# Performance work log

Hardware: AMD Instinct MI355X
Metric: run time of the kernel (lower is better)

## Reference

```python
import jax, jax.numpy as jnp
import numpy as np

B, T, D, N, L = 8, 2048, 256, 64, 4
LN_EPS = 1e-5


def setup_inputs() -> dict:
    key = jax.random.key(0)
    ks = jax.random.split(key, 8)
    def rn(k, shape, scale=1.0):
        return jax.random.normal(k, shape, dtype=jnp.float32) * scale
    A_init = jnp.log(0.5 + jnp.arange(N, dtype=jnp.float32))  # (N,)
    inp = {
        "sequences": rn(ks[0], (B, T, D)),
        # per-layer stacked params (leading dim L)
        "Wi": rn(ks[1], (L, D, D), 1.0 / np.sqrt(D)),
        "bi": jnp.zeros((L, D), jnp.float32),
        "A_log": jnp.broadcast_to(A_init, (L, D, N)) + 0.0,
        "Cm": rn(ks[2], (L, D, N), 1.0 / np.sqrt(N)),
        "Dp": jnp.ones((L, D), jnp.float32),
        "log_dt": jax.random.uniform(ks[3], (L, D), jnp.float32) * (np.log(0.1) - np.log(0.001)) + np.log(0.001),
        "Wo": rn(ks[4], (L, D, D), 1.0 / np.sqrt(D)),
        "bo": jnp.zeros((L, D), jnp.float32),
        "ln1_g": jnp.ones((L, D), jnp.float32),
        "ln1_b": jnp.zeros((L, D), jnp.float32),
        "ln2_g": jnp.ones((L, D), jnp.float32),
        "ln2_b": jnp.zeros((L, D), jnp.float32),
        "W1": rn(ks[5], (L, D, 4 * D), 1.0 / np.sqrt(D)),
        "b1": jnp.zeros((L, 4 * D), jnp.float32),
        "W2": rn(ks[6], (L, 4 * D, D), 1.0 / np.sqrt(4 * D)),
        "b2": jnp.zeros((L, D), jnp.float32),
        "lnf_g": jnp.ones((D,), jnp.float32),
        "lnf_b": jnp.zeros((D,), jnp.float32),
    }
    return inp


def _ln(x, g, b):
    m = x.mean(-1, keepdims=True)
    v = x.var(-1, keepdims=True)
    return (x - m) / jnp.sqrt(v + LN_EPS) * g + b


def _s4_kernel(A_log_l, Cm_l, log_dt_l, Tlen):
    dt = jnp.exp(log_dt_l)                       # (D,)
    A = -jnp.exp(A_log_l)                        # (D,N)
    A_bar = jnp.exp(A * dt[:, None])             # (D,N)
    B_bar = (A_bar - 1.0) / (A * np.sqrt(N))     # (D,N)
    CB = Cm_l * B_bar                            # (D,N)
    logAb = jnp.log(jnp.clip(A_bar, 1e-10))
    powers = jnp.arange(Tlen, dtype=jnp.float32)
    # (D,N,T) power tensor contracted over N -> (D,T)
    return jnp.einsum('dn,dnt->dt', CB, jnp.exp(logAb[:, :, None] * powers))


def reference(sequences, Wi, bi, A_log, Cm, Dp, log_dt, Wo, bo,
              ln1_g, ln1_b, ln2_g, ln2_b, W1, b1, W2, b2, lnf_g, lnf_b):
    x = sequences  # dropout is identity in eval mode
    Tlen = x.shape[1]
    nfft = 2 * Tlen
    for l in range(L):
        # --- S4D sub-block (pre-norm) ---
        h = _ln(x, ln1_g[l], ln1_b[l])
        u = (h @ Wi[l] + bi[l]).transpose(0, 2, 1)   # (B,D,T)
        K = _s4_kernel(A_log[l], Cm[l], log_dt[l], Tlen)  # (D,T)
        u_f = jnp.fft.rfft(u, n=nfft, axis=-1)
        K_f = jnp.fft.rfft(K, n=nfft, axis=-1)
        y = jnp.fft.irfft(u_f * K_f[None], n=nfft, axis=-1)[..., :Tlen]
        y = y + Dp[l][None, :, None] * u
        y = y.transpose(0, 2, 1) @ Wo[l] + bo[l]
        x = x + y
        # --- MLP sub-block (pre-norm) ---
        h2 = _ln(x, ln2_g[l], ln2_b[l])
        x = x + (jax.nn.gelu(h2 @ W1[l] + b1[l], approximate=False) @ W2[l] + b2[l])
    return _ln(x, lnf_g, lnf_b)
```

## Files before the change

kernel.cpp:

```cpp
#include <hip/hip_runtime.h>
#include <hip/hip_bf16.h>

#define NB 8
#define TT 2048
#define DD 256
#define NN 64
#define LL 4
#define CC 32
#define GG 64
#define BT (NB*TT)

typedef __attribute__((ext_vector_type(8))) short short8;
typedef __attribute__((ext_vector_type(4))) short short4v;
typedef __attribute__((ext_vector_type(4))) float f32x4;

__device__ __forceinline__ float bf2f(__hip_bfloat16 v){ return __bfloat162float(v); }
__device__ __forceinline__ __hip_bfloat16 f2bf(float v){ return __float2bfloat16(v); }
__device__ __forceinline__ short f2bfbits(float v){
  __hip_bfloat16 h = __float2bfloat16(v);
  return __builtin_bit_cast(short, h);
}
__device__ __forceinline__ float bfbits2f(short s){
  __hip_bfloat16 h = __builtin_bit_cast(__hip_bfloat16, s);
  return __bfloat162float(h);
}

__device__ __forceinline__ int get_bf(const void* dtp){
  unsigned u = *(const unsigned*)dtp;
  return ((u >> 16) == (u & 0xFFFFu)) ? 1 : 0;
}

__device__ __forceinline__ float ldin(const void* p, size_t i, int bf){
  return bf ? __bfloat162float(((const __hip_bfloat16*)p)[i]) : ((const float*)p)[i];
}

__device__ __forceinline__ float gelu_f(float x){
  float y = 0.79788456f * fmaf(0.044715f, x*x*x, x);
  float e = __expf(-2.0f * fabsf(y));
  float t = (1.0f - e) / (1.0f + e);
  t = (y >= 0.0f) ? t : -t;
  return 0.5f * x * (1.0f + t);
}

__device__ __forceinline__ void async16(const void* g, void* l){
  __builtin_amdgcn_global_load_lds(
      (const __attribute__((address_space(1))) void*)(unsigned long long)g,
      (__attribute__((address_space(3))) void*)(unsigned long long)l,
      16, 0, 0);
}

__global__ __launch_bounds__(256) void cast_ln_kernel(const void* __restrict__ seq,
    __hip_bfloat16* __restrict__ x, __hip_bfloat16* __restrict__ hN,
    const void* __restrict__ g, const void* __restrict__ b,
    const void* __restrict__ dtp)
{
  int bf = get_bf(dtp);
  int lane = threadIdx.x & 63, w = threadIdx.x >> 6;
  int row = blockIdx.x * 4 + w;
  int c = lane * 4;
  size_t base = (size_t)row*DD + c;
  float v0 = ldin(seq, base+0, bf), v1 = ldin(seq, base+1, bf);
  float v2 = ldin(seq, base+2, bf), v3 = ldin(seq, base+3, bf);
  short4v xk; xk.x=f2bfbits(v0); xk.y=f2bfbits(v1); xk.z=f2bfbits(v2); xk.w=f2bfbits(v3);
  *(short4v*)(x + base) = xk;
  float s = v0+v1+v2+v3;
  #pragma unroll
  for (int o = 1; o < 64; o <<= 1) s += __shfl_xor(s, o);
  float mean = s * (1.0f/DD);
  float d0=v0-mean, d1=v1-mean, d2=v2-mean, d3=v3-mean;
  float sq = d0*d0+d1*d1+d2*d2+d3*d3;
  #pragma unroll
  for (int o = 1; o < 64; o <<= 1) sq += __shfl_xor(sq, o);
  float r = rsqrtf(sq * (1.0f/DD) + 1e-5f);
  short4v hk;
  hk.x = f2bfbits(d0*r*ldin(g,c+0,bf) + ldin(b,c+0,bf));
  hk.y = f2bfbits(d1*r*ldin(g,c+1,bf) + ldin(b,c+1,bf));
  hk.z = f2bfbits(d2*r*ldin(g,c+2,bf) + ldin(b,c+2,bf));
  hk.w = f2bfbits(d3*r*ldin(g,c+3,bf) + ldin(b,c+3,bf));
  *(short4v*)(hN + base) = hk;
}

__global__ __launch_bounds__(256) void transpose_all_kernel(
    const void* __restrict__ Wi, const void* __restrict__ Wo,
    const void* __restrict__ W1, const void* __restrict__ W2,
    __hip_bfloat16* __restrict__ WiT, __hip_bfloat16* __restrict__ WoT,
    __hip_bfloat16* __restrict__ W1T, __hip_bfloat16* __restrict__ W2T,
    const void* __restrict__ dtp)
{
  int bf = get_bf(dtp);
  __shared__ float tile[32][33];
  int id = blockIdx.x;
  const void* W; __hip_bfloat16* Wt; int K, N, l, n0, k0;
  if (id < 256){
    W=Wi; Wt=WiT; K=DD; N=DD;
    int t=id;       l=t>>6; int r=t&63;  n0=(r&7)*32;  k0=(r>>3)*32;
  } else if (id < 512){
    W=Wo; Wt=WoT; K=DD; N=DD;
    int t=id-256;   l=t>>6; int r=t&63;  n0=(r&7)*32;  k0=(r>>3)*32;
  } else if (id < 1536){
    W=W1; Wt=W1T; K=DD; N=4*DD;
    int t=id-512;   l=t>>8; int r=t&255; n0=(r&31)*32; k0=(r>>5)*32;
  } else {
    W=W2; Wt=W2T; K=4*DD; N=DD;
    int t=id-1536;  l=t>>8; int r=t&255; n0=(r&7)*32;  k0=(r>>3)*32;
  }
  size_t zoff = (size_t)l * K * N;
  int tx = threadIdx.x, ty = threadIdx.y;
  #pragma unroll
  for (int i = 0; i < 4; i++)
    tile[ty + i*8][tx] = ldin(W, zoff + (size_t)(k0 + ty + i*8)*N + n0 + tx, bf);
  __syncthreads();
  #pragma unroll
  for (int i = 0; i < 4; i++)
    Wt[zoff + (size_t)(n0 + ty + i*8)*K + k0 + tx] = f2bf(tile[tx][ty + i*8]);
}

__global__ __launch_bounds__(256) void gemm_w1_kernel(
    const __hip_bfloat16* __restrict__ A, const __hip_bfloat16* __restrict__ Wt,
    const void* __restrict__ bias, size_t boff,
    __hip_bfloat16* __restrict__ C, int N, int K, const void* __restrict__ dtp)
{
  int bf = get_bf(dtp);
  __shared__ __align__(16) char smem[24576];
  short (*Als)[128][32] = (short(*)[128][32])smem;
  short (*Bls)[64][32]  = (short(*)[64][32])(smem + 16384);
  short* Cls = (short*)smem;
  int tid = threadIdx.x;
  int lane = tid & 63, w = tid >> 6;
  int quad = lane >> 4, row16 = lane & 15;
  int wm = (w >> 1) * 64, wn = (w & 1) * 32;
  int bm = blockIdx.x * 128, bn = blockIdx.y * 64;
  const short* Ag = (const short*)A + (size_t)bm * K;
  const short* Bg = (const short*)Wt + (size_t)bn * K;
  int r0 = tid >> 2, c8 = (tid & 3) * 8;
  f32x4 acc[4][2] = {};
  for (int k0 = 0; k0 < K; k0 += 64){
    #pragma unroll
    for (int kc = 0; kc < 2; kc++){
      async16(Ag + (size_t)r0*K      + k0 + kc*32 + c8, &Als[kc][r0][c8]);
      async16(Ag + (size_t)(64+r0)*K + k0 + kc*32 + c8, &Als[kc][64+r0][c8]);
      async16(Bg + (size_t)r0*K      + k0 + kc*32 + c8, &Bls[kc][r0][c8]);
    }
    __syncthreads();
    #pragma unroll
    for (int kc = 0; kc < 2; kc++){
      short8 af[4], bfr[2];
      #pragma unroll
      for (int i = 0; i < 4; i++)
        af[i] = *(const short8*)&Als[kc][wm + i*16 + row16][quad*8];
      #pragma unroll
      for (int j = 0; j < 2; j++)
        bfr[j] = *(const short8*)&Bls[kc][wn + j*16 + row16][quad*8];
      #pragma unroll
      for (int i = 0; i < 4; i++)
        #pragma unroll
        for (int j = 0; j < 2; j++)
          acc[i][j] = __builtin_amdgcn_mfma_f32_16x16x32_bf16(af[i], bfr[j], acc[i][j], 0, 0, 0);
    }
    __syncthreads();
  }
  #pragma unroll
  for (int i = 0; i < 4; i++){
    #pragma unroll
    for (int j = 0; j < 2; j++){
      int col = wn + j*16 + row16;
      float bv = ldin(bias, boff + bn + col, bf);
      #pragma unroll
      for (int r = 0; r < 4; r++){
        int row = wm + i*16 + quad*4 + r;
        Cls[row*72 + col] = f2bfbits(gelu_f(acc[i][j][r] + bv));
      }
    }
  }
  __syncthreads();
  #pragma unroll
  for (int p = 0; p < 4; p++){
    int ch = p*256 + tid;
    int row = ch >> 3, c0 = (ch & 7) * 8;
    short8 v = *(const short8*)&Cls[row*72 + c0];
    *(short8*)&C[(size_t)(bm + row)*N + bn + c0] = v;
  }
}

__global__ __launch_bounds__(256) void gemm_wi_lf_kernel(
    const __hip_bfloat16* __restrict__ A, const __hip_bfloat16* __restrict__ Wt,
    const void* __restrict__ bias, size_t boff,
    __hip_bfloat16* __restrict__ uout, __hip_bfloat16* __restrict__ LFS,
    const float* __restrict__ abT, int K, const void* __restrict__ dtp)
{
  int bf = get_bf(dtp);
  __shared__ __align__(16) char smem[73728];
  short (*Als)[32][32]  = (short(*)[32][32])smem;
  short (*Bls)[256][32] = (short(*)[256][32])(smem + 8192);
  float* Cls = (float*)smem;
  int tid = threadIdx.x, lane = tid & 63, w = tid >> 6;
  int quad = lane >> 4, row16 = lane & 15;
  int wn = w * 64;
  int bm = blockIdx.x * 32;
  const short* Ag = (const short*)A + (size_t)bm * K;
  const short* Bg = (const short*)Wt;
  f32x4 acc[2][4] = {};
  for (int k0 = 0; k0 < K; k0 += 128){
    #pragma unroll
    for (int p = 0; p < 2; p++){
      int ch = p*256 + tid;
      int kc = ch >> 7, r = (ch >> 2) & 31, c = (ch & 3) * 8;
      async16(Ag + (size_t)r*K + k0 + kc*32 + c, &Als[kc][r][c]);
    }
    #pragma unroll
    for (int p = 0; p < 16; p++){
      int ch = p*256 + tid;
      int kc = ch >> 10, r = (ch >> 2) & 255, c = (ch & 3) * 8;
      async16(Bg + (size_t)r*K + k0 + kc*32 + c, &Bls[kc][r][c]);
    }
    __syncthreads();
    #pragma unroll
    for (int kc = 0; kc < 4; kc++){
      short8 af[2], bfr[4];
      #pragma unroll
      for (int i = 0; i < 2; i++)
        af[i] = *(const short8*)&Als[kc][i*16 + row16][quad*8];
      #pragma unroll
      for (int j = 0; j < 4; j++)
        bfr[j] = *(const short8*)&Bls[kc][wn + j*16 + row16][quad*8];
      #pragma unroll
      for (int i = 0; i < 2; i++)
        #pragma unroll
        for (int j = 0; j < 4; j++)
          acc[i][j] = __builtin_amdgcn_mfma_f32_16x16x32_bf16(af[i], bfr[j], acc[i][j], 0, 0, 0);
    }
    __syncthreads();
  }
  #pragma unroll
  for (int i = 0; i < 2; i++)
    #pragma unroll
    for (int j = 0; j < 4; j++){
      int col = wn + j*16 + row16;
      #pragma unroll
      for (int r = 0; r < 4; r++){
        int row = i*16 + quad*4 + r;
        Cls[row*260 + col] = acc[i][j][r];
      }
    }
  __syncthreads();
  {
    int row = tid >> 3, l7 = tid & 7;
    size_t rbase = (size_t)(bm + row)*DD;
    #pragma unroll
    for (int q = 0; q < 8; q++){
      int c0 = l7*4 + q*32;
      float4 t = *(const float4*)&Cls[row*260 + c0];
      float v0 = t.x + ldin(bias, boff+c0+0, bf);
      float v1 = t.y + ldin(bias, boff+c0+1, bf);
      float v2 = t.z + ldin(bias, boff+c0+2, bf);
      float v3 = t.w + ldin(bias, boff+c0+3, bf);
      float4 wbk; wbk.x=v0; wbk.y=v1; wbk.z=v2; wbk.w=v3;
      *(float4*)&Cls[row*260 + c0] = wbk;
      short4v pk; pk.x=f2bfbits(v0); pk.y=f2bfbits(v1); pk.z=f2bfbits(v2); pk.w=f2bfbits(v3);
      *(short4v*)&uout[rbase + c0] = pk;
    }
  }
  __syncthreads();
  {
    int d = tid;
    int cix = bm >> 5;
    float ab[NN], accn[NN];
    #pragma unroll
    for (int n = 0; n < NN; n++){ ab[n] = abT[n*DD + d]; accn[n] = 0.0f; }
    #pragma unroll 1
    for (int s = 0; s < CC; s++){
      float uv = Cls[s*260 + d];
      #pragma unroll
      for (int n = 0; n < NN; n++) accn[n] = fmaf(ab[n], accn[n], uv);
    }
    #pragma unroll
    for (int n = 0; n < NN; n++)
      LFS[((size_t)cix*NN + n)*DD + d] = f2bf(accn[n]);
  }
}

__global__ __launch_bounds__(256) void s4_scan_kernel(__hip_bfloat16* __restrict__ LFS,
    const float* __restrict__ AbarCT)
{
  int d = threadIdx.x;
  int n = blockIdx.x & (NN-1), b = blockIdx.x >> 6;
  float a = AbarCT[n*DD + d];
  size_t base = ((size_t)(b*GG)*NN + n)*DD + d;
  const size_t gs = (size_t)NN*DD;
  float s = 0.0f;
  #pragma unroll 1
  for (int g = 0; g < GG; g += 4){
    size_t i0 = base + (size_t)(g+0)*gs;
    size_t i1 = base + (size_t)(g+1)*gs;
    size_t i2 = base + (size_t)(g+2)*gs;
    size_t i3 = base + (size_t)(g+3)*gs;
    float lf0 = bf2f(LFS[i0]);
    float lf1 = bf2f(LFS[i1]);
    float lf2 = bf2f(LFS[i2]);
    float lf3 = bf2f(LFS[i3]);
    LFS[i0] = f2bf(s); s = fmaf(a, s, lf0);
    LFS[i1] = f2bf(s); s = fmaf(a, s, lf1);
    LFS[i2] = f2bf(s); s = fmaf(a, s, lf2);
    LFS[i3] = f2bf(s); s = fmaf(a, s, lf3);
  }
}

__global__ __launch_bounds__(512, 4) void gemm_wo_recur_kernel(
    const __hip_bfloat16* __restrict__ uB, const __hip_bfloat16* __restrict__ Sin,
    const float* __restrict__ abT, const float* __restrict__ cbT,
    const void* __restrict__ Dp, size_t dpoff,
    const __hip_bfloat16* __restrict__ Wt, const void* __restrict__ bias, size_t boff,
    const __hip_bfloat16* __restrict__ resx, __hip_bfloat16* __restrict__ xout,
    const void* __restrict__ g, size_t goff, const void* __restrict__ bb, size_t bboff,
    __hip_bfloat16* __restrict__ hout, int K)
{
  int bf = get_bf(Dp);
  __shared__ __align__(16) char smem[65536];
  short* Uls   = (short*)smem;
  short* Afull = (short*)(smem + 16384);
  short (*Bls)[256][32] = (short(*)[256][32])(smem + 32768);
  float* Cls = (float*)smem;
  int tid = threadIdx.x, lane = tid & 63, w = tid >> 6;
  int quad = lane >> 4, row16 = lane & 15;
  int bm = blockIdx.x * 32;
  {
    const short* ug = (const short*)uB + (size_t)bm * DD;
    async16(ug + tid*8,        Uls + tid*8);
    async16(ug + 4096 + tid*8, Uls + 4096 + tid*8);
  }
  int d = tid >> 1, ng = tid & 1, nb = ng * 32;
  float st[32], ab[32], cb[32];
  {
    const __hip_bfloat16* sbase = Sin + ((size_t)(bm >> 5) * NN + nb)*DD + d;
    const float* abase = abT + (size_t)nb*DD + d;
    const float* cbase = cbT + (size_t)nb*DD + d;
    #pragma unroll
    for (int i = 0; i < 32; i++){
      st[i] = bf2f(sbase[(size_t)i*DD]);
      ab[i] = abase[(size_t)i*DD];
      cb[i] = cbase[(size_t)i*DD];
    }
  }
  float dp = ldin(Dp, dpoff + d, bf);
  __syncthreads();
  {
    short* ya = Afull + (d >> 5)*1024 + (d & 31);
    #pragma unroll 1
    for (int tau = 0; tau < CC; tau++){
      float uv = bfbits2f(Uls[tau*DD + d]);
      float a0 = 0.0f, a1 = 0.0f, a2 = 0.0f, a3 = 0.0f;
      #pragma unroll
      for (int i = 0; i < 32; i += 4){
        st[i+0] = fmaf(ab[i+0], st[i+0], uv); a0 = fmaf(cb[i+0], st[i+0], a0);
        st[i+1] = fmaf(ab[i+1], st[i+1], uv); a1 = fmaf(cb[i+1], st[i+1], a1);
        st[i+2] = fmaf(ab[i+2], st[i+2], uv); a2 = fmaf(cb[i+2], st[i+2], a2);
        st[i+3] = fmaf(ab[i+3], st[i+3], uv); a3 = fmaf(cb[i+3], st[i+3], a3);
      }
      float tot = (a0 + a1) + (a2 + a3);
      tot += __shfl_xor(tot, 1);
      if (ng == 0) ya[tau*32] = f2bfbits(fmaf(dp, uv, tot));
    }
  }
  __syncthreads();
  const short* Bg = (const short*)Wt;
  int wn = w * 32;
  f32x4 acc[2][2] = {};
  for (int k0 = 0; k0 < K; k0 += 64){
    #pragma unroll
    for (int p = 0; p < 4; p++){
      int ch = p*512 + tid;
      int kc = ch >> 10, rem = ch & 1023, r = rem >> 2, c = (rem & 3) * 8;
      async16(Bg + (size_t)r*K + k0 + kc*32 + c, &Bls[kc][r][c]);
    }
    __syncthreads();
    #pragma unroll
    for (int kc = 0; kc < 2; kc++){
      short8 af[2], bfr[2];
      #pragma unroll
      for (int i = 0; i < 2; i++)
        af[i] = *(const short8*)&Afull[((k0 >> 5) + kc)*1024 + (i*16 + row16)*32 + quad*8];
      #pragma unroll
      for (int j = 0; j < 2; j++)
        bfr[j] = *(const short8*)&Bls[kc][wn + j*16 + row16][quad*8];
      #pragma unroll
      for (int i = 0; i < 2; i++)
        #pragma unroll
        for (int j = 0; j < 2; j++)
          acc[i][j] = __builtin_amdgcn_mfma_f32_16x16x32_bf16(af[i], bfr[j], acc[i][j], 0, 0, 0);
    }
    __syncthreads();
  }
  #pragma unroll
  for (int i = 0; i < 2; i++)
    #pragma unroll
    for (int j = 0; j < 2; j++){
      int col = wn + j*16 + row16;
      #pragma unroll
      for (int r = 0; r < 4; r++){
        int row = i*16 + quad*4 + r;
        Cls[row*260 + col] = acc[i][j][r];
      }
    }
  __syncthreads();
  int row = tid >> 4, l4 = tid & 15;
  size_t rbase = (size_t)(bm + row)*DD;
  float v[4][4];
  #pragma unroll
  for (int q = 0; q < 4; q++){
    int c0 = l4*4 + q*64;
    float4 t = *(const float4*)&Cls[row*260 + c0];
    short4v rx = *(const short4v*)&resx[rbase + c0];
    v[q][0] = t.x + ldin(bias, boff+c0+0, bf) + bfbits2f(rx.x);
    v[q][1] = t.y + ldin(bias, boff+c0+1, bf) + bfbits2f(rx.y);
    v[q][2] = t.z + ldin(bias, boff+c0+2, bf) + bfbits2f(rx.z);
    v[q][3] = t.w + ldin(bias, boff+c0+3, bf) + bfbits2f(rx.w);
    short4v pk; pk.x=f2bfbits(v[q][0]); pk.y=f2bfbits(v[q][1]);
    pk.z=f2bfbits(v[q][2]); pk.w=f2bfbits(v[q][3]);
    *(short4v*)&xout[rbase + c0] = pk;
  }
  float s = 0.0f, sq = 0.0f;
  #pragma unroll
  for (int q = 0; q < 4; q++)
    #pragma unroll
    for (int e = 0; e < 4; e++){ s += v[q][e]; sq += v[q][e]*v[q][e]; }
  #pragma unroll
  for (int o = 1; o < 16; o <<= 1){ s += __shfl_xor(s, o); sq += __shfl_xor(sq, o); }
  float mean = s * (1.0f/DD);
  float rstd = rsqrtf(sq * (1.0f/DD) - mean*mean + 1e-5f);
  #pragma unroll
  for (int q = 0; q < 4; q++){
    int c0 = l4*4 + q*64;
    short4v pk;
    pk.x = f2bfbits((v[q][0]-mean)*rstd*ldin(g,goff+c0+0,bf) + ldin(bb,bboff+c0+0,bf));
    pk.y = f2bfbits((v[q][1]-mean)*rstd*ldin(g,goff+c0+1,bf) + ldin(bb,bboff+c0+1,bf));
    pk.z = f2bfbits((v[q][2]-mean)*rstd*ldin(g,goff+c0+2,bf) + ldin(bb,bboff+c0+2,bf));
    pk.w = f2bfbits((v[q][3]-mean)*rstd*ldin(g,goff+c0+3,bf) + ldin(bb,bboff+c0+3,bf));
    *(short4v*)&hout[rbase + c0] = pk;
  }
}

template <int MODE>
__global__ __launch_bounds__(256) void gemm_row_kernel(
    const __hip_bfloat16* __restrict__ A, const __hip_bfloat16* __restrict__ Wt,
    const void* __restrict__ bias, size_t boff,
    const __hip_bfloat16* __restrict__ resx, __hip_bfloat16* __restrict__ xout,
    const void* __restrict__ g, size_t goff,
    const void* __restrict__ bb, size_t bboff,
    __hip_bfloat16* __restrict__ hout, void* __restrict__ vout,
    int K, const void* __restrict__ dtp)
{
  int bf = get_bf(dtp);
  __shared__ __align__(16) char smem[73728];
  short (*Als)[32][32]  = (short(*)[32][32])smem;
  short (*Bls)[256][32] = (short(*)[256][32])(smem + 8192);
  float* Cls = (float*)smem;
  int tid = threadIdx.x, lane = tid & 63, w = tid >> 6;
  int quad = lane >> 4, row16 = lane & 15;
  int wn = w * 64;
  int bm = blockIdx.x * 32;
  const short* Ag = (const short*)A + (size_t)bm * K;
  const short* Bg = (const short*)Wt;
  f32x4 acc[2][4] = {};
  for (int k0 = 0; k0 < K; k0 += 128){
    #pragma unroll
    for (int p = 0; p < 2; p++){
      int ch = p*256 + tid;
      int kc = ch >> 7, r = (ch >> 2) & 31, c = (ch & 3) * 8;
      async16(Ag + (size_t)r*K + k0 + kc*32 + c, &Als[kc][r][c]);
    }
    #pragma unroll
    for (int p = 0; p < 16; p++){
      int ch = p*256 + tid;
      int kc = ch >> 10, r = (ch >> 2) & 255, c = (ch & 3) * 8;
      async16(Bg + (size_t)r*K + k0 + kc*32 + c, &Bls[kc][r][c]);
    }
    __syncthreads();
    #pragma unroll
    for (int kc = 0; kc < 4; kc++){
      short8 af[2], bfr[4];
      #pragma unroll
      for (int i = 0; i < 2; i++)
        af[i] = *(const short8*)&Als[kc][i*16 + row16][quad*8];
      #pragma unroll
      for (int j = 0; j < 4; j++)
        bfr[j] = *(const short8*)&Bls[kc][wn + j*16 + row16][quad*8];
      #pragma unroll
      for (int i = 0; i < 2; i++)
        #pragma unroll
        for (int j = 0; j < 4; j++)
          acc[i][j] = __builtin_amdgcn_mfma_f32_16x16x32_bf16(af[i], bfr[j], acc[i][j], 0, 0, 0);
    }
    __syncthreads();
  }
  #pragma unroll
  for (int i = 0; i < 2; i++)
    #pragma unroll
    for (int j = 0; j < 4; j++){
      int col = wn + j*16 + row16;
      #pragma unroll
      for (int r = 0; r < 4; r++){
        int row = i*16 + quad*4 + r;
        Cls[row*260 + col] = acc[i][j][r];
      }
    }
  __syncthreads();
  int row = tid >> 3, l7 = tid & 7;
  size_t rbase = (size_t)(bm + row)*DD;
  float v[8][4];
  #pragma unroll
  for (int q = 0; q < 8; q++){
    int c0 = l7*4 + q*32;
    float4 t = *(const float4*)&Cls[row*260 + c0];
    short4v rx = *(const short4v*)&resx[rbase + c0];
    v[q][0] = t.x + ldin(bias, boff+c0+0, bf) + bfbits2f(rx.x);
    v[q][1] = t.y + ldin(bias, boff+c0+1, bf) + bfbits2f(rx.y);
    v[q][2] = t.z + ldin(bias, boff+c0+2, bf) + bfbits2f(rx.z);
    v[q][3] = t.w + ldin(bias, boff+c0+3, bf) + bfbits2f(rx.w);
    if (MODE == 1){
      short4v pk; pk.x=f2bfbits(v[q][0]); pk.y=f2bfbits(v[q][1]);
      pk.z=f2bfbits(v[q][2]); pk.w=f2bfbits(v[q][3]);
      *(short4v*)&xout[rbase + c0] = pk;
    }
  }
  float s = 0.0f, sq = 0.0f;
  #pragma unroll
  for (int q = 0; q < 8; q++)
    #pragma unroll
    for (int e = 0; e < 4; e++){ s += v[q][e]; sq += v[q][e]*v[q][e]; }
  #pragma unroll
  for (int o = 1; o < 8; o <<= 1){ s += __shfl_xor(s, o); sq += __shfl_xor(sq, o); }
  float mean = s * (1.0f/DD);
  float rstd = rsqrtf(sq * (1.0f/DD) - mean*mean + 1e-5f);
  #pragma unroll
  for (int q = 0; q < 8; q++){
    int c0 = l7*4 + q*32;
    float o0 = (v[q][0]-mean)*rstd*ldin(g,goff+c0+0,bf) + ldin(bb,bboff+c0+0,bf);
    float o1 = (v[q][1]-mean)*rstd*ldin(g,goff+c0+1,bf) + ldin(bb,bboff+c0+1,bf);
    float o2 = (v[q][2]-mean)*rstd*ldin(g,goff+c0+2,bf) + ldin(bb,bboff+c0+2,bf);
    float o3 = (v[q][3]-mean)*rstd*ldin(g,goff+c0+3,bf) + ldin(bb,bboff+c0+3,bf);
    if (MODE == 1){
      short4v pk; pk.x=f2bfbits(o0); pk.y=f2bfbits(o1); pk.z=f2bfbits(o2); pk.w=f2bfbits(o3);
      *(short4v*)&hout[rbase + c0] = pk;
    } else {
      if (bf){
        short4v pk; pk.x=f2bfbits(o0); pk.y=f2bfbits(o1); pk.z=f2bfbits(o2); pk.w=f2bfbits(o3);
        *(short4v*)&((__hip_bfloat16*)vout)[rbase + c0] = pk;
      } else {
        float4 pk; pk.x=o0; pk.y=o1; pk.z=o2; pk.w=o3;
        *(float4*)&((float*)vout)[rbase + c0] = pk;
      }
    }
  }
}

__global__ __launch_bounds__(256) void s4_setup_kernel(const void* __restrict__ A_log,
    const void* __restrict__ Cm, const void* __restrict__ log_dt,
    float* __restrict__ AbarT, float* __restrict__ AbarCT, float* __restrict__ cbT,
    const void* __restrict__ dtp)
{
  int bf = get_bf(dtp);
  int d = threadIdx.x, n = blockIdx.x, l = blockIdx.y;
  float dtv = expf(ldin(log_dt, (size_t)l*DD + d, bf));
  float A   = -expf(ldin(A_log, ((size_t)l*DD + d)*NN + n, bf));
  float ab  = expf(A * dtv);
  float bbv = (fabsf(A) > 1e-8f) ? (ab - 1.0f) / (A * 8.0f) : dtv * 0.125f;
  float cb  = ldin(Cm, ((size_t)l*DD + d)*NN + n, bf) * bbv;
  size_t o = ((size_t)l*NN + n)*DD + d;
  AbarT[o] = ab;
  cbT[o]   = cb;
  float p = ab;
  #pragma unroll
  for (int i = 0; i < 5; i++) p *= p;
  AbarCT[o] = p;
}

extern "C" void kernel_launch(void* const* d_in, const int* in_sizes, int n_in,
                              void* d_out, int out_size, void* d_ws, size_t ws_size,
                              hipStream_t stream) {
  const void* seq   = d_in[0];
  const void* Wi    = d_in[1];
  const void* bi    = d_in[2];
  const void* A_log = d_in[3];
  const void* Cm    = d_in[4];
  const void* Dp    = d_in[5];
  const void* logdt = d_in[6];
  const void* Wo    = d_in[7];
  const void* bo    = d_in[8];
  const void* ln1g  = d_in[9];
  const void* ln1b  = d_in[10];
  const void* ln2g  = d_in[11];
  const void* ln2b  = d_in[12];
  const void* W1    = d_in[13];
  const void* b1    = d_in[14];
  const void* W2    = d_in[15];
  const void* b2    = d_in[16];
  const void* lnfg  = d_in[17];
  const void* lnfb  = d_in[18];

  char* ws = (char*)d_ws;
  size_t off = 0;
  __hip_bfloat16* x   = (__hip_bfloat16*)(ws + off); off += (size_t)BT*DD*2;
  __hip_bfloat16* uB  = (__hip_bfloat16*)(ws + off); off += (size_t)BT*DD*2;
  __hip_bfloat16* hN  = (__hip_bfloat16*)(ws + off); off += (size_t)BT*DD*2;
  __hip_bfloat16* mid = (__hip_bfloat16*)(ws + off); off += (size_t)BT*4*DD*2;
  __hip_bfloat16* LFS = (__hip_bfloat16*)(ws + off); off += (size_t)NB*GG*NN*DD*2;
  __hip_bfloat16* WiT = (__hip_bfloat16*)(ws + off); off += (size_t)LL*DD*DD*2;
  __hip_bfloat16* WoT = (__hip_bfloat16*)(ws + off); off += (size_t)LL*DD*DD*2;
  __hip_bfloat16* W1T = (__hip_bfloat16*)(ws + off); off += (size_t)LL*DD*4*DD*2;
  __hip_bfloat16* W2T = (__hip_bfloat16*)(ws + off); off += (size_t)LL*4*DD*DD*2;
  float* AbarT  = (float*)(ws + off); off += (size_t)LL*NN*DD*4;
  float* AbarCT = (float*)(ws + off); off += (size_t)LL*NN*DD*4;
  float* cbT    = (float*)(ws + off); off += (size_t)LL*NN*DD*4;

  (void)in_sizes; (void)n_in; (void)out_size; (void)ws_size;

  cast_ln_kernel<<<BT/4, 256, 0, stream>>>(seq, x, hN, ln1g, ln1b, Dp);
  transpose_all_kernel<<<2560, dim3(32,8), 0, stream>>>(
      Wi, Wo, W1, W2, WiT, WoT, W1T, W2T, Dp);
  s4_setup_kernel<<<dim3(NN, LL), DD, 0, stream>>>(A_log, Cm, logdt, AbarT, AbarCT, cbT, Dp);

  for (int l = 0; l < LL; l++){
    const size_t oD  = (size_t)l*DD;
    const size_t o4D = (size_t)l*4*DD;
    const float* abT  = AbarT  + (size_t)l*NN*DD;
    const float* abCT = AbarCT + (size_t)l*NN*DD;
    const float* cbTl = cbT    + (size_t)l*NN*DD;

    gemm_wi_lf_kernel<<<BT/32, 256, 0, stream>>>(
        hN, WiT + (size_t)l*DD*DD, bi, oD, uB, LFS, abT, DD, Dp);
    s4_scan_kernel<<<NB*NN, 256, 0, stream>>>(LFS, abCT);
    gemm_wo_recur_kernel<<<BT/32, 512, 0, stream>>>(
        uB, LFS, abT, cbTl, Dp, oD,
        WoT + (size_t)l*DD*DD, bo, oD, x, x,
        ln2g, oD, ln2b, oD, hN, DD);

    gemm_w1_kernel<<<dim3(BT/128, 4*DD/64), 256, 0, stream>>>(
        hN, W1T + (size_t)l*DD*4*DD, b1, o4D, mid, 4*DD, DD, Dp);
    if (l < LL-1){
      gemm_row_kernel<1><<<BT/32, 256, 0, stream>>>(
          mid, W2T + (size_t)l*4*DD*DD, b2, oD, x, x,
          ln1g, (size_t)(l+1)*DD, ln1b, (size_t)(l+1)*DD, hN, nullptr, 4*DD, Dp);
    } else {
      gemm_row_kernel<2><<<BT/32, 256, 0, stream>>>(
          mid, W2T + (size_t)l*4*DD*DD, b2, oD, x, nullptr,
          lnfg, 0, lnfb, 0, nullptr, d_out, 4*DD, Dp);
    }
  }
}
```

Measured before the change: 616.7 us.

## Split fused recurrence+Wo GEMM into separate recurrence and row-GEMM kernels

Unfuses the chunked S4 recurrence from the Wo projection. The recurrence kernel now writes y to a global scratch buffer (reusing the mid buffer), and the existing gemm_row_kernel<1> does Wo, bias, residual and LN2. The goal is to shrink the recurrence kernel's shared memory (only the U tile remains) so more blocks can run at once, and to reuse the tuned GEMM path. The cost is an extra kernel launch plus a global round trip of y.

```diff
diff --git a/kernel.cpp b/kernel.cpp
--- a/kernel.cpp
+++ b/kernel.cpp
@@ -305,24 +305,16 @@
   }
 }
 
-__global__ __launch_bounds__(512, 4) void gemm_wo_recur_kernel(
+__global__ __launch_bounds__(512, 4) void recur_kernel(
     const __hip_bfloat16* __restrict__ uB, const __hip_bfloat16* __restrict__ Sin,
     const float* __restrict__ abT, const float* __restrict__ cbT,
     const void* __restrict__ Dp, size_t dpoff,
-    const __hip_bfloat16* __restrict__ Wt, const void* __restrict__ bias, size_t boff,
-    const __hip_bfloat16* __restrict__ resx, __hip_bfloat16* __restrict__ xout,
-    const void* __restrict__ g, size_t goff, const void* __restrict__ bb, size_t bboff,
-    __hip_bfloat16* __restrict__ hout, int K)
+    __hip_bfloat16* __restrict__ yout)
 {
   int bf = get_bf(Dp);
-  __shared__ __align__(16) char smem[65536];
-  short* Uls   = (short*)smem;
-  short* Afull = (short*)(smem + 16384);
-  short (*Bls)[256][32] = (short(*)[256][32])(smem + 32768);
-  float* Cls = (float*)smem;
-  int tid = threadIdx.x, lane = tid & 63, w = tid >> 6;
-  int quad = lane >> 4, row16 = lane & 15;
-  int bm = blockIdx.x * 32;
+  __shared__ __align__(16) short Uls[CC*DD];
+  int tid = threadIdx.x;
+  int bm = blockIdx.x * CC;
   {
     const short* ug = (const short*)uB + (size_t)bm * DD;
     async16(ug + tid*8,        Uls + tid*8);
@@ -343,99 +335,23 @@
   }
   float dp = ldin(Dp, dpoff + d, bf);
   __syncthreads();
-  {
-    short* ya = Afull + (d >> 5)*1024 + (d & 31);
-    #pragma unroll 1
-    for (int tau = 0; tau < CC; tau++){
-      float uv = bfbits2f(Uls[tau*DD + d]);
-      float a0 = 0.0f, a1 = 0.0f, a2 = 0.0f, a3 = 0.0f;
-      #pragma unroll
-      for (int i = 0; i < 32; i += 4){
-        st[i+0] = fmaf(ab[i+0], st[i+0], uv); a0 = fmaf(cb[i+0], st[i+0], a0);
-        st[i+1] = fmaf(ab[i+1], st[i+1], uv); a1 = fmaf(cb[i+1], st[i+1], a1);
-        st[i+2] = fmaf(ab[i+2], st[i+2], uv); a2 = fmaf(cb[i+2], st[i+2], a2);
-        st[i+3] = fmaf(ab[i+3], st[i+3], uv); a3 = fmaf(cb[i+3], st[i+3], a3);
-      }
-      float tot = (a0 + a1) + (a2 + a3);
-      tot += __shfl_xor(tot, 1);
-      if (ng == 0) ya[tau*32] = f2bfbits(fmaf(dp, uv, tot));
-    }
-  }
-  __syncthreads();
-  const short* Bg = (const short*)Wt;
-  int wn = w * 32;
-  f32x4 acc[2][2] = {};
-  for (int k0 = 0; k0 < K; k0 += 64){
-    #pragma unroll
-    for (int p = 0; p < 4; p++){
-      int ch = p*512 + tid;
-      int kc = ch >> 10, rem = ch & 1023, r = rem >> 2, c = (rem & 3) * 8;
-      async16(Bg + (size_t)r*K + k0 + kc*32 + c, &Bls[kc][r][c]);
-    }
-    __syncthreads();
-    #pragma unroll
-    for (int kc = 0; kc < 2; kc++){
-      short8 af[2], bfr[2];
-      #pragma unroll
-      for (int i = 0; i < 2; i++)
-        af[i] = *(const short8*)&Afull[((k0 >> 5) + kc)*1024 + (i*16 + row16)*32 + quad*8];
-      #pragma unroll
-      for (int j = 0; j < 2; j++)
-        bfr[j] = *(const short8*)&Bls[kc][wn + j*16 + row16][quad*8];
-      #pragma unroll
-      for (int i = 0; i < 2; i++)
-        #pragma unroll
-        for (int j = 0; j < 2; j++)
-          acc[i][j] = __builtin_amdgcn_mfma_f32_16x16x32_bf16(af[i], bfr[j], acc[i][j], 0, 0, 0);
-    }
-    __syncthreads();
-  }
-  #pragma unroll
-  for (int i = 0; i < 2; i++)
-    #pragma unroll
-    for (int j = 0; j < 2; j++){
-      int col = wn + j*16 + row16;
-      #pragma unroll
-      for (int r = 0; r < 4; r++){
-        int row = i*16 + quad*4 + r;
-        Cls[row*260 + col] = acc[i][j][r];
-      }
-    }
-  __syncthreads();
-  int row = tid >> 4, l4 = tid & 15;
-  size_t rbase = (size_t)(bm + row)*DD;
-  float v[4][4];
-  #pragma unroll
-  for (int q = 0; q < 4; q++){
-    int c0 = l4*4 + q*64;
-    float4 t = *(const float4*)&Cls[row*260 + c0];
-    short4v rx = *(const short4v*)&resx[rbase + c0];
-    v[q][0] = t.x + ldin(bias, boff+c0+0, bf) + bfbits2f(rx.x);
-    v[q][1] = t.y + ldin(bias, boff+c0+1, bf) + bfbits2f(rx.y);
-    v[q][2] = t.z + ldin(bias, boff+c0+2, bf) + bfbits2f(rx.z);
-    v[q][3] = t.w + ldin(bias, boff+c0+3, bf) + bfbits2f(rx.w);
-    short4v pk; pk.x=f2bfbits(v[q][0]); pk.y=f2bfbits(v[q][1]);
-    pk.z=f2bfbits(v[q][2]); pk.w=f2bfbits(v[q][3]);
-    *(short4v*)&xout[rbase + c0] = pk;
-  }
-  float s = 0.0f, sq = 0.0f;
-  #pragma unroll
-  for (int q = 0; q < 4; q++)
-    #pragma unroll
-    for (int e = 0; e < 4; e++){ s += v[q][e]; sq += v[q][e]*v[q][e]; }
-  #pragma unroll
-  for (int o = 1; o < 16; o <<= 1){ s += __shfl_xor(s, o); sq += __shfl_xor(sq, o); }
-  float mean = s * (1.0f/DD);
-  float rstd = rsqrtf(sq * (1.0f/DD) - mean*mean + 1e-5f);
-  #pragma unroll
-  for (int q = 0; q < 4; q++){
-    int c0 = l4*4 + q*64;
-    short4v pk;
-    pk.x = f2bfbits((v[q][0]-mean)*rstd*ldin(g,goff+c0+0,bf) + ldin(bb,bboff+c0+0,bf));
-    pk.y = f2bfbits((v[q][1]-mean)*rstd*ldin(g,goff+c0+1,bf) + ldin(bb,bboff+c0+1,bf));
-    pk.z = f2bfbits((v[q][2]-mean)*rstd*ldin(g,goff+c0+2,bf) + ldin(bb,bboff+c0+2,bf));
-    pk.w = f2bfbits((v[q][3]-mean)*rstd*ldin(g,goff+c0+3,bf) + ldin(bb,bboff+c0+3,bf));
-    *(short4v*)&hout[rbase + c0] = pk;
+  __hip_bfloat16* ya = yout + (size_t)bm*DD + d;
+  float uv = bfbits2f(Uls[d]);
+  #pragma unroll 1
+  for (int tau = 0; tau < CC; tau++){
+    float uvn = (tau < CC-1) ? bfbits2f(Uls[(tau+1)*DD + d]) : 0.0f;
+    float a0 = 0.0f, a1 = 0.0f, a2 = 0.0f, a3 = 0.0f;
+    #pragma unroll
+    for (int i = 0; i < 32; i += 4){
+      st[i+0] = fmaf(ab[i+0], st[i+0], uv); a0 = fmaf(cb[i+0], st[i+0], a0);
+      st[i+1] = fmaf(ab[i+1], st[i+1], uv); a1 = fmaf(cb[i+1], st[i+1], a1);
+      st[i+2] = fmaf(ab[i+2], st[i+2], uv); a2 = fmaf(cb[i+2], st[i+2], a2);
+      st[i+3] = fmaf(ab[i+3], st[i+3], uv); a3 = fmaf(cb[i+3], st[i+3], a3);
+    }
+    float tot = (a0 + a1) + (a2 + a3);
+    tot += __shfl_xor(tot, 1);
+    if (ng == 0) ya[(size_t)tau*DD] = f2bf(fmaf(dp, uv, tot));
+    uv = uvn;
   }
 }
 
@@ -612,6 +528,8 @@
   float* AbarCT = (float*)(ws + off); off += (size_t)LL*NN*DD*4;
   float* cbT    = (float*)(ws + off); off += (size_t)LL*NN*DD*4;
 
+  __hip_bfloat16* yC = mid;
+
   (void)in_sizes; (void)n_in; (void)out_size; (void)ws_size;
 
   cast_ln_kernel<<<BT/4, 256, 0, stream>>>(seq, x, hN, ln1g, ln1b, Dp);
@@ -629,10 +547,11 @@
     gemm_wi_lf_kernel<<<BT/32, 256, 0, stream>>>(
         hN, WiT + (size_t)l*DD*DD, bi, oD, uB, LFS, abT, DD, Dp);
     s4_scan_kernel<<<NB*NN, 256, 0, stream>>>(LFS, abCT);
-    gemm_wo_recur_kernel<<<BT/32, 512, 0, stream>>>(
-        uB, LFS, abT, cbTl, Dp, oD,
-        WoT + (size_t)l*DD*DD, bo, oD, x, x,
-        ln2g, oD, ln2b, oD, hN, DD);
+    recur_kernel<<<BT/32, 512, 0, stream>>>(
+        uB, LFS, abT, cbTl, Dp, oD, yC);
+    gemm_row_kernel<1><<<BT/32, 256, 0, stream>>>(
+        yC, WoT + (size_t)l*DD*DD, bo, oD, x, x,
+        ln2g, oD, ln2b, oD, hN, nullptr, DD, Dp);
 
     gemm_w1_kernel<<<dim3(BT/128, 4*DD/64), 256, 0, stream>>>(
         hN, W1T + (size_t)l*DD*4*DD, b1, o4D, mid, 4*DD, DD, Dp);
```

Result: slower. 643.0 us (+4.3%).

## Double-buffer GEMM k-tiles and prefetch Wo tiles during the scan recurrence

Applied to the files above, without the earlier changes.

The Wi and W2 row GEMMs now use ping-pong LDS buffers with 64-wide k-tiles, so the loads for tile t+1 are issued while tile t is computed. The Wo GEMM inside the recurrence kernel loads its first weight tile during the scan and then alternates between the freed U buffer and a new buffer. Its LDS footprint shrinks, which may let more blocks fit per CU. The scan loop also prefetches the next u value one step ahead. The cost is more barrier iterations with less work between them.

```diff
diff --git a/kernel.cpp b/kernel.cpp
--- a/kernel.cpp
+++ b/kernel.cpp
@@ -190,8 +190,8 @@
 {
   int bf = get_bf(dtp);
   __shared__ __align__(16) char smem[73728];
-  short (*Als)[32][32]  = (short(*)[32][32])smem;
-  short (*Bls)[256][32] = (short(*)[256][32])(smem + 8192);
+  short (*Als)[2][32][32]  = (short(*)[2][32][32])smem;
+  short (*Bls)[2][256][32] = (short(*)[2][256][32])(smem + 8192);
   float* Cls = (float*)smem;
   int tid = threadIdx.x, lane = tid & 63, w = tid >> 6;
   int quad = lane >> 4, row16 = lane & 15;
@@ -199,30 +199,39 @@
   int bm = blockIdx.x * 32;
   const short* Ag = (const short*)A + (size_t)bm * K;
   const short* Bg = (const short*)Wt;
+  int nt = K >> 6;
+  {
+    int ch = tid; int kc = ch>>7, r=(ch>>2)&31, c=(ch&3)*8;
+    async16(Ag + (size_t)r*K + kc*32 + c, &Als[0][kc][r][c]);
+    #pragma unroll
+    for (int p = 0; p < 8; p++){
+      int c2 = p*256 + tid; int k2 = c2>>10, r2=(c2>>2)&255, cc=(c2&3)*8;
+      async16(Bg + (size_t)r2*K + k2*32 + cc, &Bls[0][k2][r2][cc]);
+    }
+  }
+  __syncthreads();
   f32x4 acc[2][4] = {};
-  for (int k0 = 0; k0 < K; k0 += 128){
-    #pragma unroll
-    for (int p = 0; p < 2; p++){
-      int ch = p*256 + tid;
-      int kc = ch >> 7, r = (ch >> 2) & 31, c = (ch & 3) * 8;
-      async16(Ag + (size_t)r*K + k0 + kc*32 + c, &Als[kc][r][c]);
-    }
-    #pragma unroll
-    for (int p = 0; p < 16; p++){
-      int ch = p*256 + tid;
-      int kc = ch >> 10, r = (ch >> 2) & 255, c = (ch & 3) * 8;
-      async16(Bg + (size_t)r*K + k0 + kc*32 + c, &Bls[kc][r][c]);
-    }
-    __syncthreads();
-    #pragma unroll
-    for (int kc = 0; kc < 4; kc++){
+  for (int t = 0; t < nt; t++){
+    int cur = t & 1;
+    if (t + 1 < nt){
+      int nb_ = cur ^ 1, k0 = (t+1) << 6;
+      int ch = tid; int kc = ch>>7, r=(ch>>2)&31, c=(ch&3)*8;
+      async16(Ag + (size_t)r*K + k0 + kc*32 + c, &Als[nb_][kc][r][c]);
+      #pragma unroll
+      for (int p = 0; p < 8; p++){
+        int c2 = p*256 + tid; int k2 = c2>>10, r2=(c2>>2)&255, cc=(c2&3)*8;
+        async16(Bg + (size_t)r2*K + k0 + k2*32 + cc, &Bls[nb_][k2][r2][cc]);
+      }
+    }
+    #pragma unroll
+    for (int kc = 0; kc < 2; kc++){
       short8 af[2], bfr[4];
       #pragma unroll
       for (int i = 0; i < 2; i++)
-        af[i] = *(const short8*)&Als[kc][i*16 + row16][quad*8];
+        af[i] = *(const short8*)&Als[cur][kc][i*16 + row16][quad*8];
       #pragma unroll
       for (int j = 0; j < 4; j++)
-        bfr[j] = *(const short8*)&Bls[kc][wn + j*16 + row16][quad*8];
+        bfr[j] = *(const short8*)&Bls[cur][kc][wn + j*16 + row16][quad*8];
       #pragma unroll
       for (int i = 0; i < 2; i++)
         #pragma unroll
@@ -312,21 +321,27 @@
     const __hip_bfloat16* __restrict__ Wt, const void* __restrict__ bias, size_t boff,
     const __hip_bfloat16* __restrict__ resx, __hip_bfloat16* __restrict__ xout,
     const void* __restrict__ g, size_t goff, const void* __restrict__ bb, size_t bboff,
-    __hip_bfloat16* __restrict__ hout, int K)
+    __hip_bfloat16* __restrict__ hout)
 {
   int bf = get_bf(Dp);
-  __shared__ __align__(16) char smem[65536];
+  __shared__ __align__(16) char smem[50176];
   short* Uls   = (short*)smem;
   short* Afull = (short*)(smem + 16384);
-  short (*Bls)[256][32] = (short(*)[256][32])(smem + 32768);
-  float* Cls = (float*)smem;
+  short* Bext  = (short*)(smem + 32768);
+  float* Cls   = (float*)(smem + 16384);
   int tid = threadIdx.x, lane = tid & 63, w = tid >> 6;
   int quad = lane >> 4, row16 = lane & 15;
-  int bm = blockIdx.x * 32;
+  int bm = blockIdx.x * CC;
+  const short* Bg = (const short*)Wt;
   {
     const short* ug = (const short*)uB + (size_t)bm * DD;
     async16(ug + tid*8,        Uls + tid*8);
     async16(ug + 4096 + tid*8, Uls + 4096 + tid*8);
+    #pragma unroll
+    for (int p = 0; p < 2; p++){
+      int ch = p*512 + tid; int r = ch >> 2, c = (ch & 3) * 8;
+      async16(Bg + (size_t)r*DD + c, Bext + ch*8);
+    }
   }
   int d = tid >> 1, ng = tid & 1, nb = ng * 32;
   float st[32], ab[32], cb[32];
@@ -345,9 +360,10 @@
   __syncthreads();
   {
     short* ya = Afull + (d >> 5)*1024 + (d & 31);
+    float uv = bfbits2f(Uls[d]);
     #pragma unroll 1
     for (int tau = 0; tau < CC; tau++){
-      float uv = bfbits2f(Uls[tau*DD + d]);
+      float uvn = (tau < CC-1) ? bfbits2f(Uls[(tau+1)*DD + d]) : 0.0f;
       float a0 = 0.0f, a1 = 0.0f, a2 = 0.0f, a3 = 0.0f;
       #pragma unroll
       for (int i = 0; i < 32; i += 4){
@@ -359,35 +375,35 @@
       float tot = (a0 + a1) + (a2 + a3);
       tot += __shfl_xor(tot, 1);
       if (ng == 0) ya[tau*32] = f2bfbits(fmaf(dp, uv, tot));
-    }
-  }
-  __syncthreads();
-  const short* Bg = (const short*)Wt;
+      uv = uvn;
+    }
+  }
+  __syncthreads();
   int wn = w * 32;
   f32x4 acc[2][2] = {};
-  for (int k0 = 0; k0 < K; k0 += 64){
-    #pragma unroll
-    for (int p = 0; p < 4; p++){
-      int ch = p*512 + tid;
-      int kc = ch >> 10, rem = ch & 1023, r = rem >> 2, c = (rem & 3) * 8;
-      async16(Bg + (size_t)r*K + k0 + kc*32 + c, &Bls[kc][r][c]);
-    }
-    __syncthreads();
-    #pragma unroll
-    for (int kc = 0; kc < 2; kc++){
-      short8 af[2], bfr[2];
-      #pragma unroll
-      for (int i = 0; i < 2; i++)
-        af[i] = *(const short8*)&Afull[((k0 >> 5) + kc)*1024 + (i*16 + row16)*32 + quad*8];
+  #pragma unroll
+  for (int t = 0; t < 8; t++){
+    if (t < 7){
+      short* nxt = ((t+1) & 1) ? Uls : Bext;
+      #pragma unroll
+      for (int p = 0; p < 2; p++){
+        int ch = p*512 + tid; int r = ch >> 2, c = (ch & 3) * 8;
+        async16(Bg + (size_t)r*DD + (t+1)*32 + c, nxt + ch*8);
+      }
+    }
+    const short* cur = (t & 1) ? Uls : Bext;
+    short8 af[2], bfr[2];
+    #pragma unroll
+    for (int i = 0; i < 2; i++)
+      af[i] = *(const short8*)&Afull[t*1024 + (i*16 + row16)*32 + quad*8];
+    #pragma unroll
+    for (int j = 0; j < 2; j++)
+      bfr[j] = *(const short8*)&cur[(wn + j*16 + row16)*32 + quad*8];
+    #pragma unroll
+    for (int i = 0; i < 2; i++)
       #pragma unroll
       for (int j = 0; j < 2; j++)
-        bfr[j] = *(const short8*)&Bls[kc][wn + j*16 + row16][quad*8];
-      #pragma unroll
-      for (int i = 0; i < 2; i++)
-        #pragma unroll
-        for (int j = 0; j < 2; j++)
-          acc[i][j] = __builtin_amdgcn_mfma_f32_16x16x32_bf16(af[i], bfr[j], acc[i][j], 0, 0, 0);
-    }
+        acc[i][j] = __builtin_amdgcn_mfma_f32_16x16x32_bf16(af[i], bfr[j], acc[i][j], 0, 0, 0);
     __syncthreads();
   }
   #pragma unroll
@@ -451,8 +467,8 @@
 {
   int bf = get_bf(dtp);
   __shared__ __align__(16) char smem[73728];
-  short (*Als)[32][32]  = (short(*)[32][32])smem;
-  short (*Bls)[256][32] = (short(*)[256][32])(smem + 8192);
+  short (*Als)[2][32][32]  = (short(*)[2][32][32])smem;
+  short (*Bls)[2][256][32] = (short(*)[2][256][32])(smem + 8192);
   float* Cls = (float*)smem;
   int tid = threadIdx.x, lane = tid & 63, w = tid >> 6;
   int quad = lane >> 4, row16 = lane & 15;
@@ -460,30 +476,39 @@
   int bm = blockIdx.x * 32;
   const short* Ag = (const short*)A + (size_t)bm * K;
   const short* Bg = (const short*)Wt;
+  int nt = K >> 6;
+  {
+    int ch = tid; int kc = ch>>7, r=(ch>>2)&31, c=(ch&3)*8;
+    async16(Ag + (size_t)r*K + kc*32 + c, &Als[0][kc][r][c]);
+    #pragma unroll
+    for (int p = 0; p < 8; p++){
+      int c2 = p*256 + tid; int k2 = c2>>10, r2=(c2>>2)&255, cc=(c2&3)*8;
+      async16(Bg + (size_t)r2*K + k2*32 + cc, &Bls[0][k2][r2][cc]);
+    }
+  }
+  __syncthreads();
   f32x4 acc[2][4] = {};
-  for (int k0 = 0; k0 < K; k0 += 128){
-    #pragma unroll
-    for (int p = 0; p < 2; p++){
-      int ch = p*256 + tid;
-      int kc = ch >> 7, r = (ch >> 2) & 31, c = (ch & 3) * 8;
-      async16(Ag + (size_t)r*K + k0 + kc*32 + c, &Als[kc][r][c]);
-    }
-    #pragma unroll
-    for (int p = 0; p < 16; p++){
-      int ch = p*256 + tid;
-      int kc = ch >> 10, r = (ch >> 2) & 255, c = (ch & 3) * 8;
-      async16(Bg + (size_t)r*K + k0 + kc*32 + c, &Bls[kc][r][c]);
-    }
-    __syncthreads();
-    #pragma unroll
-    for (int kc = 0; kc < 4; kc++){
+  for (int t = 0; t < nt; t++){
+    int cur = t & 1;
+    if (t + 1 < nt){
+      int nb_ = cur ^ 1, k0 = (t+1) << 6;
+      int ch = tid; int kc = ch>>7, r=(ch>>2)&31, c=(ch&3)*8;
+      async16(Ag + (size_t)r*K + k0 + kc*32 + c, &Als[nb_][kc][r][c]);
+      #pragma unroll
+      for (int p = 0; p < 8; p++){
+        int c2 = p*256 + tid; int k2 = c2>>10, r2=(c2>>2)&255, cc=(c2&3)*8;
+        async16(Bg + (size_t)r2*K + k0 + k2*32 + cc, &Bls[nb_][k2][r2][cc]);
+      }
+    }
+    #pragma unroll
+    for (int kc = 0; kc < 2; kc++){
       short8 af[2], bfr[4];
       #pragma unroll
       for (int i = 0; i < 2; i++)
-        af[i] = *(const short8*)&Als[kc][i*16 + row16][quad*8];
+        af[i] = *(const short8*)&Als[cur][kc][i*16 + row16][quad*8];
       #pragma unroll
       for (int j = 0; j < 4; j++)
-        bfr[j] = *(const short8*)&Bls[kc][wn + j*16 + row16][quad*8];
+        bfr[j] = *(const short8*)&Bls[cur][kc][wn + j*16 + row16][quad*8];
       #pragma unroll
       for (int i = 0; i < 2; i++)
         #pragma unroll
@@ -632,7 +657,7 @@
     gemm_wo_recur_kernel<<<BT/32, 512, 0, stream>>>(
         uB, LFS, abT, cbTl, Dp, oD,
         WoT + (size_t)l*DD*DD, bo, oD, x, x,
-        ln2g, oD, ln2b, oD, hN, DD);
+        ln2g, oD, ln2b, oD, hN);
 
     gemm_w1_kernel<<<dim3(BT/128, 4*DD/64), 256, 0, stream>>>(
         hN, W1T + (size_t)l*DD*4*DD, b1, o4D, mid, 4*DD, DD, Dp);
```

New measurement: 591.2 us. 1.04x faster.
